# Optimization experiments

Hardware: AMD Instinct MI355X
Metric: run time of the kernel (lower is better)

Reference implementation:

```python
import jax, jax.numpy as jnp
import numpy as np

N = 50000
E = 800000
D_IN, D_HID, D_OUT = 256, 256, 128


def _xavier(key, shape):
    fan_in, fan_out = shape
    limit = float(np.sqrt(6.0 / (fan_in + fan_out)))
    return jax.random.uniform(key, shape, jnp.float32, -limit, limit)


def setup_inputs() -> dict:
    key = jax.random.key(0)
    ks = jax.random.split(key, 12)
    x = jax.random.normal(ks[0], (N, D_IN), jnp.float32)
    edge_index = jax.random.randint(ks[1], (2, E), 0, N, dtype=jnp.int64)
    batch = jnp.zeros((N,), jnp.int64)
    # per-layer: message weight W, linear weight LW (stored [in, out]), bias b
    w1 = _xavier(ks[2], (D_IN, D_HID))
    lw1 = _xavier(ks[3], (D_IN, D_HID))
    lb1 = jnp.zeros((D_HID,), jnp.float32)
    w2 = _xavier(ks[4], (D_HID, D_HID))
    lw2 = _xavier(ks[5], (D_HID, D_HID))
    lb2 = jnp.zeros((D_HID,), jnp.float32)
    w3 = _xavier(ks[6], (D_HID, D_OUT))
    lw3 = _xavier(ks[7], (D_HID, D_OUT))
    lb3 = jnp.zeros((D_OUT,), jnp.float32)
    return {"x": x, "edge_index": edge_index, "batch": batch,
            "w1": w1, "lw1": lw1, "lb1": lb1,
            "w2": w2, "lw2": lw2, "lb2": lb2,
            "w3": w3, "lw3": lw3, "lb3": lb3}


def _gcn_layer(x, W, LW, b, row, col, norm):
    # message: norm * (x_j @ W); equivalent and cheaper: transform nodes once, gather
    xw = x @ W                                   # [N, out]
    msg = norm[:, None] * xw[row]                # [E, out]
    agg = jax.ops.segment_sum(msg, col, num_segments=x.shape[0])  # scatter-add at col
    return agg + x @ LW + b                      # residual linear path


def reference(x, edge_index, batch, w1, lw1, lb1, w2, lw2, lb2, w3, lw3, lb3):
    row, col = edge_index[0], edge_index[1]
    ones = jnp.ones((row.shape[0],), x.dtype)
    out_deg = jax.ops.segment_sum(ones, row, num_segments=N)
    in_deg = jax.ops.segment_sum(ones, col, num_segments=N)
    # inf at zero-degree nodes never gets gathered (those nodes have no edges)
    norm = out_deg[row] ** -0.5 * in_deg[col] ** -0.5  # [E]

    h = jax.nn.relu(_gcn_layer(x, w1, lw1, lb1, row, col, norm))
    h = jax.nn.relu(_gcn_layer(h, w2, lw2, lb2, row, col, norm))
    h = jax.nn.sigmoid(_gcn_layer(h, w3, lw3, lb3, row, col, norm))
    return h
```

## Files before the change

kernel.cpp:

```cpp
#include <hip/hip_runtime.h>
#include <hip/hip_bf16.h>
#include <math.h>

#define NNODES 50000
#define NEDGES 800000
#define HNB 128
#define HBINS 50176
#define SCAN_NB 196

typedef short s8v __attribute__((ext_vector_type(8)));
typedef float f4v __attribute__((ext_vector_type(4)));
using bf16 = __hip_bfloat16;

static __device__ __forceinline__ float bf2f(unsigned int u16) {
    union { unsigned int i; float f; } c; c.i = u16 << 16; return c.f;
}


__global__ void k_packb(const float* __restrict__ W, const float* __restrict__ LW,
                        bf16* __restrict__ out, int K, int C) {
    int i = blockIdx.x * blockDim.x + threadIdx.x;
    int C2 = 2 * C;
    if (i >= K * C2) return;
    int k = i / C2, j = i % C2;
    float v = (j < C) ? W[k * C + j] : LW[k * C + (j - C)];
    out[i] = __float2bfloat16(v);
}


__global__ __launch_bounds__(256) void k_hist(const int* __restrict__ ei, ushort* __restrict__ partials) {
    __shared__ unsigned int h32[HBINS / 2];
    int b = blockIdx.x, row = blockIdx.y, t = threadIdx.x;
    for (int i = t; i < HBINS / 2; i += 256) h32[i] = 0;
    __syncthreads();
    const int chunk = NEDGES / HNB;
    int beg = b * chunk, end = beg + chunk;
    const int* p = ei + (size_t)row * NEDGES;
    for (int e = beg + t; e < end; e += 256) {
        int id = p[e];
        atomicAdd(&h32[id >> 1], 1u << (16 * (id & 1)));
    }
    __syncthreads();
    unsigned int* o32 = (unsigned int*)(partials + ((size_t)row * HNB + b) * HBINS);
    for (int i = t; i < HBINS / 2; i += 256) o32[i] = h32[i];
}

__global__ __launch_bounds__(256) void k_hist_reduce(const ushort* __restrict__ partials,
                                                     float* __restrict__ rsqrt_out,
                                                     int* __restrict__ in_cnt,
                                                     int* __restrict__ block_sums) {
    __shared__ int sm[256];
    int row = blockIdx.y;
    int i = blockIdx.x * 256 + threadIdx.x;
    const ushort* p = partials + (size_t)row * HNB * HBINS + i;
    int s = 0;
#pragma unroll 4
    for (int b = 0; b < HNB; ++b) s += p[(size_t)b * HBINS];
    if (row == 0) {
        if (i < NNODES) rsqrt_out[i] = rsqrtf((float)s);
    } else {
        if (i < NNODES) in_cnt[i] = s;
        sm[threadIdx.x] = s;
        __syncthreads();
        for (int off = 128; off > 0; off >>= 1) {
            if (threadIdx.x < off) sm[threadIdx.x] += sm[threadIdx.x + off];
            __syncthreads();
        }
        if (threadIdx.x == 0) block_sums[blockIdx.x] = sm[0];
    }
}


__global__ void k_scan_blocks(const int* __restrict__ block_sums, int* __restrict__ block_base, int nb) {
    __shared__ int s[256];
    int t = threadIdx.x;
    int v = (t < nb) ? block_sums[t] : 0;
    s[t] = v;
    __syncthreads();
    for (int off = 1; off < 256; off <<= 1) {
        int u = (t >= off) ? s[t - off] : 0;
        __syncthreads();
        s[t] += u;
        __syncthreads();
    }
    block_base[t] = s[t] - v;
}

__global__ void k_scan_final(const int* __restrict__ in_cnt, const int* __restrict__ block_base,
                             int* __restrict__ offsets, int* __restrict__ cursor) {
    __shared__ int s[256];
    int b = blockIdx.x, t = threadIdx.x;
    int i = b * 256 + t;
    int v = (i < NNODES) ? in_cnt[i] : 0;
    s[t] = v;
    __syncthreads();
    for (int off = 1; off < 256; off <<= 1) {
        int u = (t >= off) ? s[t - off] : 0;
        __syncthreads();
        s[t] += u;
        __syncthreads();
    }
    int excl = s[t] - v + block_base[b];
    if (i < NNODES) { offsets[i] = excl; cursor[i] = excl; }
    if (i == NNODES - 1) offsets[NNODES] = excl + v;
}

__global__ void k_scatter(const int* __restrict__ ei, int* __restrict__ cursor,
                          int* __restrict__ src_sorted) {
    int e = blockIdx.x * blockDim.x + threadIdx.x;
    if (e < NEDGES) {
        int r = ei[e], c = ei[NEDGES + e];
        int p = atomicAdd(&cursor[c], 1);
        src_sorted[p] = r;
    }
}

template<int D, int C2, int ACT>
__global__ void k_agg_fused(const bf16* __restrict__ xwcat, const int* __restrict__ offsets,
                            const int* __restrict__ src_sorted, const float* __restrict__ rsqrt_out,
                            const float* __restrict__ bias, void* __restrict__ out) {
    const int L = D / 8;
    const int G = 64 / L;
    int lane = threadIdx.x & 63;
    int v = blockIdx.x * (blockDim.x >> 6) + (threadIdx.x >> 6);
    if (v >= NNODES) return;
    int g = lane / L, sl = lane % L;

    float accA[8], accB[8];
#pragma unroll
    for (int c = 0; c < 8; ++c) { accA[c] = 0.f; accB[c] = 0.f; }

    int beg = offsets[v], end = offsets[v + 1];
    const ushort* base = (const ushort*)xwcat + sl * 8;
    for (int j = beg + g; j < end; j += 2 * G) {
        int s = src_sorted[j];
        float w = rsqrt_out[s];
        uint4 q = *(const uint4*)(base + (size_t)s * C2);
        accA[0] += w * bf2f(q.x & 0xffffu); accA[1] += w * bf2f(q.x >> 16);
        accA[2] += w * bf2f(q.y & 0xffffu); accA[3] += w * bf2f(q.y >> 16);
        accA[4] += w * bf2f(q.z & 0xffffu); accA[5] += w * bf2f(q.z >> 16);
        accA[6] += w * bf2f(q.w & 0xffffu); accA[7] += w * bf2f(q.w >> 16);
        int jB = j + G;
        if (jB < end) {
            int s2 = src_sorted[jB];
            float w2 = rsqrt_out[s2];
            uint4 p = *(const uint4*)(base + (size_t)s2 * C2);
            accB[0] += w2 * bf2f(p.x & 0xffffu); accB[1] += w2 * bf2f(p.x >> 16);
            accB[2] += w2 * bf2f(p.y & 0xffffu); accB[3] += w2 * bf2f(p.y >> 16);
            accB[4] += w2 * bf2f(p.z & 0xffffu); accB[5] += w2 * bf2f(p.z >> 16);
            accB[6] += w2 * bf2f(p.w & 0xffffu); accB[7] += w2 * bf2f(p.w >> 16);
        }
    }
#pragma unroll
    for (int c = 0; c < 8; ++c) accA[c] += accB[c];
#pragma unroll
    for (int d = 32; d >= L; d >>= 1) {
#pragma unroll
        for (int c = 0; c < 8; ++c) accA[c] += __shfl_down(accA[c], d, 64);
    }

    if (lane < L) {
        float sc = (end > beg) ? rsqrtf((float)(end - beg)) : 0.f;
        const ushort* lwp = (const ushort*)xwcat + (size_t)v * C2 + D + sl * 8;
        uint4 ql = *(const uint4*)lwp;
        const float* bp = bias + sl * 8;
        float4 b0 = *(const float4*)bp, b1 = *(const float4*)(bp + 4);
        float h[8];
        h[0] = accA[0] * sc + bf2f(ql.x & 0xffffu) + b0.x;
        h[1] = accA[1] * sc + bf2f(ql.x >> 16)     + b0.y;
        h[2] = accA[2] * sc + bf2f(ql.y & 0xffffu) + b0.z;
        h[3] = accA[3] * sc + bf2f(ql.y >> 16)     + b0.w;
        h[4] = accA[4] * sc + bf2f(ql.z & 0xffffu) + b1.x;
        h[5] = accA[5] * sc + bf2f(ql.z >> 16)     + b1.y;
        h[6] = accA[6] * sc + bf2f(ql.w & 0xffffu) + b1.z;
        h[7] = accA[7] * sc + bf2f(ql.w >> 16)     + b1.w;
        if (ACT == 1) {
            union { bf16 hh[8]; uint4 u; } o;
#pragma unroll
            for (int c = 0; c < 8; ++c) o.hh[c] = __float2bfloat16(fmaxf(h[c], 0.f));
            *(uint4*)((ushort*)out + (size_t)v * D + sl * 8) = o.u;
        } else {
            float r[8];
#pragma unroll
            for (int c = 0; c < 8; ++c) r[c] = 1.f / (1.f + expf(-h[c]));
            float* op = (float*)out + (size_t)v * D + sl * 8;
            *(float4*)op = (float4){r[0], r[1], r[2], r[3]};
            *(float4*)(op + 4) = (float4){r[4], r[5], r[6], r[7]};
        }
    }
}

template<int C2, bool A_BF16>
__global__ __launch_bounds__(256) void k_gemm_fused(const void* __restrict__ Aptr,
                                                    const bf16* __restrict__ B,
                                                    bf16* __restrict__ Out) {
    __shared__ bf16 As[64][40];
    __shared__ bf16 Bs[128][40];
    const int R = NNODES;
    int t = threadIdx.x;
    int wave = t >> 6, lane = t & 63;
    int r0 = blockIdx.x * 64;
    int n0 = blockIdx.y * 128;

    f4v acc[8];
#pragma unroll
    for (int i = 0; i < 8; ++i) acc[i] = (f4v){0.f, 0.f, 0.f, 0.f};

    int arow = t >> 2, aseg = t & 3;
    int bn = t & 127, bhalf = t >> 7;

    for (int k0 = 0; k0 < 256; k0 += 32) {
        {
            union { bf16 h[8]; uint4 v; } u;
            int gr = r0 + arow;
            if (gr < R) {
                if (A_BF16) {
                    const bf16* Ab = (const bf16*)Aptr;
                    u.v = *(const uint4*)(Ab + (size_t)gr * 256 + k0 + aseg * 8);
                } else {
                    const float* Af = (const float*)Aptr;
                    const float4* p = (const float4*)(Af + (size_t)gr * 256 + k0 + aseg * 8);
                    float4 f0 = p[0], f1 = p[1];
                    u.h[0] = __float2bfloat16(f0.x); u.h[1] = __float2bfloat16(f0.y);
                    u.h[2] = __float2bfloat16(f0.z); u.h[3] = __float2bfloat16(f0.w);
                    u.h[4] = __float2bfloat16(f1.x); u.h[5] = __float2bfloat16(f1.y);
                    u.h[6] = __float2bfloat16(f1.z); u.h[7] = __float2bfloat16(f1.w);
                }
            } else {
                u.v = (uint4){0, 0, 0, 0};
            }
            *(uint4*)&As[arow][aseg * 8] = u.v;
        }
        {
#pragma unroll
            for (int s8 = 0; s8 < 2; ++s8) {
                int kseg = bhalf * 2 + s8;
                union { bf16 h[8]; uint4 v; } u;
#pragma unroll
                for (int j = 0; j < 8; ++j)
                    u.h[j] = B[(size_t)(k0 + kseg * 8 + j) * C2 + n0 + bn];
                *(uint4*)&Bs[bn][kseg * 8] = u.v;
            }
        }
        __syncthreads();
        int m = wave * 16 + (lane & 15);
        int kq = (lane >> 4) * 8;
        s8v a = *(const s8v*)&As[m][kq];
#pragma unroll
        for (int nt = 0; nt < 8; ++nt) {
            s8v b = *(const s8v*)&Bs[nt * 16 + (lane & 15)][kq];
            acc[nt] = __builtin_amdgcn_mfma_f32_16x16x32_bf16(a, b, acc[nt], 0, 0, 0);
        }
        __syncthreads();
    }
#pragma unroll
    for (int nt = 0; nt < 8; ++nt) {
#pragma unroll
        for (int r = 0; r < 4; ++r) {
            int grow = r0 + wave * 16 + (lane >> 4) * 4 + r;
            int gcol = n0 + nt * 16 + (lane & 15);
            if (grow < R)
                Out[(size_t)grow * C2 + gcol] = __float2bfloat16(acc[nt][r]);
        }
    }
}


extern "C" void kernel_launch(void* const* d_in, const int* in_sizes, int n_in,
                              void* d_out, int out_size, void* d_ws, size_t ws_size,
                              hipStream_t stream) {
    const float* x   = (const float*)d_in[0];
    const int*   ei  = (const int*)d_in[1];
    const float* w1  = (const float*)d_in[3];
    const float* lw1 = (const float*)d_in[4];
    const float* lb1 = (const float*)d_in[5];
    const float* w2  = (const float*)d_in[6];
    const float* lw2 = (const float*)d_in[7];
    const float* lb2 = (const float*)d_in[8];
    const float* w3  = (const float*)d_in[9];
    const float* lw3 = (const float*)d_in[10];
    const float* lb3 = (const float*)d_in[11];
    float* out = (float*)d_out;

    char* ws = (char*)d_ws;
    size_t off = 0;
    auto alloc = [&](size_t bytes) -> void* {
        void* p = ws + off;
        off += (bytes + 255) & ~(size_t)255;
        return p;
    };
    int*    in_cnt     = (int*)alloc((size_t)HBINS * 4);
    float*  rsqrt_out  = (float*)alloc((size_t)HBINS * 4);
    int*    offsets    = (int*)alloc((size_t)(NNODES + 1) * 4);
    int*    cursor     = (int*)alloc((size_t)NNODES * 4);
    int*    block_sums = (int*)alloc((size_t)256 * 4);
    int*    block_base = (int*)alloc((size_t)256 * 4);
    ushort* partials   = (ushort*)alloc((size_t)2 * HNB * HBINS * 2);
    int*    src_sorted = (int*)alloc((size_t)NEDGES * 4);
    bf16*   wcat1      = (bf16*)alloc((size_t)256 * 512 * 2);
    bf16*   wcat2      = (bf16*)alloc((size_t)256 * 512 * 2);
    bf16*   wcat3      = (bf16*)alloc((size_t)256 * 256 * 2);
    bf16*   xwcat      = (bf16*)alloc((size_t)NNODES * 512 * 2);
    bf16*   h1         = (bf16*)alloc((size_t)NNODES * 256 * 2);
    bf16*   h2         = (bf16*)alloc((size_t)NNODES * 256 * 2);

    k_packb<<<512, 256, 0, stream>>>(w1, lw1, wcat1, 256, 256);
    k_packb<<<512, 256, 0, stream>>>(w2, lw2, wcat2, 256, 256);
    k_packb<<<256, 256, 0, stream>>>(w3, lw3, wcat3, 256, 128);

    k_hist<<<dim3(HNB, 2), 256, 0, stream>>>(ei, partials);
    k_hist_reduce<<<dim3(SCAN_NB, 2), 256, 0, stream>>>(partials, rsqrt_out, in_cnt, block_sums);
    k_scan_blocks<<<1, 256, 0, stream>>>(block_sums, block_base, SCAN_NB);
    k_scan_final<<<SCAN_NB, 256, 0, stream>>>(in_cnt, block_base, offsets, cursor);
    int eblocks = (NEDGES + 255) / 256;
    k_scatter<<<eblocks, 256, 0, stream>>>(ei, cursor, src_sorted);

    int gx = (NNODES + 63) / 64;
    int ablocks = NNODES / 4;

    k_gemm_fused<512, false><<<dim3(gx, 4), 256, 0, stream>>>(x, wcat1, xwcat);
    k_agg_fused<256, 512, 1><<<ablocks, 256, 0, stream>>>(xwcat, offsets, src_sorted, rsqrt_out, lb1, h1);
    k_gemm_fused<512, true><<<dim3(gx, 4), 256, 0, stream>>>(h1, wcat2, xwcat);
    k_agg_fused<256, 512, 1><<<ablocks, 256, 0, stream>>>(xwcat, offsets, src_sorted, rsqrt_out, lb2, h2);
    k_gemm_fused<256, true><<<dim3(gx, 2), 256, 0, stream>>>(h2, wcat3, xwcat);
    k_agg_fused<128, 256, 2><<<ablocks, 256, 0, stream>>>(xwcat, offsets, src_sorted, rsqrt_out, lb3, out);
}
```

Baseline: 457.3 us.

## Preload neighbor ids per wave and unroll gather with shuffle broadcast

The aggregation kernel now runs one 64-thread wave per node. Each lane loads up to 64 neighbor ids and their weights once, then broadcasts them with shuffles inside a 4-way unrolled gather loop, with a scalar tail loop for degrees above 64. This removes the serialized dependent index-then-weight loads from the inner loop and adds memory-level parallelism. The bf16 high-half unpack now uses a mask instead of a shift. In exchange it launches many small blocks and does wasted predicated loads (weight zero, reading row of id 0) when the degree is not a multiple of the unrolled stride.

```diff
diff --git a/kernel.cpp b/kernel.cpp
--- a/kernel.cpp
+++ b/kernel.cpp
@@ -12,8 +12,11 @@
 typedef float f4v __attribute__((ext_vector_type(4)));
 using bf16 = __hip_bfloat16;
 
-static __device__ __forceinline__ float bf2f(unsigned int u16) {
-    union { unsigned int i; float f; } c; c.i = u16 << 16; return c.f;
+static __device__ __forceinline__ float bflo(unsigned int x) {
+    union { unsigned int i; float f; } c; c.i = x << 16; return c.f;
+}
+static __device__ __forceinline__ float bfhi(unsigned int x) {
+    union { unsigned int i; float f; } c; c.i = x & 0xffff0000u; return c.f;
 }
 
 
@@ -116,64 +119,84 @@
 }
 
 template<int D, int C2, int ACT>
-__global__ void k_agg_fused(const bf16* __restrict__ xwcat, const int* __restrict__ offsets,
-                            const int* __restrict__ src_sorted, const float* __restrict__ rsqrt_out,
-                            const float* __restrict__ bias, void* __restrict__ out) {
+__global__ __launch_bounds__(64) void k_agg_fused(const bf16* __restrict__ xwcat,
+                                                  const int* __restrict__ offsets,
+                                                  const int* __restrict__ src_sorted,
+                                                  const float* __restrict__ rsqrt_out,
+                                                  const float* __restrict__ bias,
+                                                  void* __restrict__ out) {
     const int L = D / 8;
     const int G = 64 / L;
-    int lane = threadIdx.x & 63;
-    int v = blockIdx.x * (blockDim.x >> 6) + (threadIdx.x >> 6);
-    if (v >= NNODES) return;
+    const int U = 4;
+    int lane = threadIdx.x;
+    int v = blockIdx.x;
     int g = lane / L, sl = lane % L;
 
-    float accA[8], accB[8];
-#pragma unroll
-    for (int c = 0; c < 8; ++c) { accA[c] = 0.f; accB[c] = 0.f; }
-
     int beg = offsets[v], end = offsets[v + 1];
+    int deg = end - beg;
+    int dcap = min(deg, 64);
+
+    int id = 0; float wl = 0.f;
+    if (lane < dcap) {
+        id = src_sorted[beg + lane];
+        wl = rsqrt_out[id];
+    }
+
+    float acc[U][8];
+#pragma unroll
+    for (int u = 0; u < U; ++u)
+#pragma unroll
+        for (int c = 0; c < 8; ++c) acc[u][c] = 0.f;
+
     const ushort* base = (const ushort*)xwcat + sl * 8;
-    for (int j = beg + g; j < end; j += 2 * G) {
+
+    for (int e0 = 0; e0 < dcap; e0 += G * U) {
+#pragma unroll
+        for (int u = 0; u < U; ++u) {
+            int e = e0 + u * G + g;
+            int s = __shfl(id, e & 63, 64);
+            float w = __shfl(wl, e & 63, 64);
+            if (e >= dcap) w = 0.f;
+            uint4 q = *(const uint4*)(base + (size_t)s * C2);
+            acc[u][0] += w * bflo(q.x); acc[u][1] += w * bfhi(q.x);
+            acc[u][2] += w * bflo(q.y); acc[u][3] += w * bfhi(q.y);
+            acc[u][4] += w * bflo(q.z); acc[u][5] += w * bfhi(q.z);
+            acc[u][6] += w * bflo(q.w); acc[u][7] += w * bfhi(q.w);
+        }
+    }
+    for (int j = beg + 64 + g; j < end; j += G) {
         int s = src_sorted[j];
         float w = rsqrt_out[s];
         uint4 q = *(const uint4*)(base + (size_t)s * C2);
-        accA[0] += w * bf2f(q.x & 0xffffu); accA[1] += w * bf2f(q.x >> 16);
-        accA[2] += w * bf2f(q.y & 0xffffu); accA[3] += w * bf2f(q.y >> 16);
-        accA[4] += w * bf2f(q.z & 0xffffu); accA[5] += w * bf2f(q.z >> 16);
-        accA[6] += w * bf2f(q.w & 0xffffu); accA[7] += w * bf2f(q.w >> 16);
-        int jB = j + G;
-        if (jB < end) {
-            int s2 = src_sorted[jB];
-            float w2 = rsqrt_out[s2];
-            uint4 p = *(const uint4*)(base + (size_t)s2 * C2);
-            accB[0] += w2 * bf2f(p.x & 0xffffu); accB[1] += w2 * bf2f(p.x >> 16);
-            accB[2] += w2 * bf2f(p.y & 0xffffu); accB[3] += w2 * bf2f(p.y >> 16);
-            accB[4] += w2 * bf2f(p.z & 0xffffu); accB[5] += w2 * bf2f(p.z >> 16);
-            accB[6] += w2 * bf2f(p.w & 0xffffu); accB[7] += w2 * bf2f(p.w >> 16);
-        }
-    }
-#pragma unroll
-    for (int c = 0; c < 8; ++c) accA[c] += accB[c];
+        acc[0][0] += w * bflo(q.x); acc[0][1] += w * bfhi(q.x);
+        acc[0][2] += w * bflo(q.y); acc[0][3] += w * bfhi(q.y);
+        acc[0][4] += w * bflo(q.z); acc[0][5] += w * bfhi(q.z);
+        acc[0][6] += w * bflo(q.w); acc[0][7] += w * bfhi(q.w);
+    }
+
+#pragma unroll
+    for (int c = 0; c < 8; ++c) acc[0][c] = (acc[0][c] + acc[1][c]) + (acc[2][c] + acc[3][c]);
 #pragma unroll
     for (int d = 32; d >= L; d >>= 1) {
 #pragma unroll
-        for (int c = 0; c < 8; ++c) accA[c] += __shfl_down(accA[c], d, 64);
+        for (int c = 0; c < 8; ++c) acc[0][c] += __shfl_down(acc[0][c], d, 64);
     }
 
     if (lane < L) {
-        float sc = (end > beg) ? rsqrtf((float)(end - beg)) : 0.f;
+        float sc = (deg > 0) ? rsqrtf((float)deg) : 0.f;
         const ushort* lwp = (const ushort*)xwcat + (size_t)v * C2 + D + sl * 8;
         uint4 ql = *(const uint4*)lwp;
         const float* bp = bias + sl * 8;
         float4 b0 = *(const float4*)bp, b1 = *(const float4*)(bp + 4);
         float h[8];
-        h[0] = accA[0] * sc + bf2f(ql.x & 0xffffu) + b0.x;
-        h[1] = accA[1] * sc + bf2f(ql.x >> 16)     + b0.y;
-        h[2] = accA[2] * sc + bf2f(ql.y & 0xffffu) + b0.z;
-        h[3] = accA[3] * sc + bf2f(ql.y >> 16)     + b0.w;
-        h[4] = accA[4] * sc + bf2f(ql.z & 0xffffu) + b1.x;
-        h[5] = accA[5] * sc + bf2f(ql.z >> 16)     + b1.y;
-        h[6] = accA[6] * sc + bf2f(ql.w & 0xffffu) + b1.z;
-        h[7] = accA[7] * sc + bf2f(ql.w >> 16)     + b1.w;
+        h[0] = acc[0][0] * sc + bflo(ql.x) + b0.x;
+        h[1] = acc[0][1] * sc + bfhi(ql.x) + b0.y;
+        h[2] = acc[0][2] * sc + bflo(ql.y) + b0.z;
+        h[3] = acc[0][3] * sc + bfhi(ql.y) + b0.w;
+        h[4] = acc[0][4] * sc + bflo(ql.z) + b1.x;
+        h[5] = acc[0][5] * sc + bfhi(ql.z) + b1.y;
+        h[6] = acc[0][6] * sc + bflo(ql.w) + b1.z;
+        h[7] = acc[0][7] * sc + bfhi(ql.w) + b1.w;
         if (ACT == 1) {
             union { bf16 hh[8]; uint4 u; } o;
 #pragma unroll
@@ -316,12 +339,11 @@
     k_scatter<<<eblocks, 256, 0, stream>>>(ei, cursor, src_sorted);
 
     int gx = (NNODES + 63) / 64;
-    int ablocks = NNODES / 4;
 
     k_gemm_fused<512, false><<<dim3(gx, 4), 256, 0, stream>>>(x, wcat1, xwcat);
-    k_agg_fused<256, 512, 1><<<ablocks, 256, 0, stream>>>(xwcat, offsets, src_sorted, rsqrt_out, lb1, h1);
+    k_agg_fused<256, 512, 1><<<NNODES, 64, 0, stream>>>(xwcat, offsets, src_sorted, rsqrt_out, lb1, h1);
     k_gemm_fused<512, true><<<dim3(gx, 4), 256, 0, stream>>>(h1, wcat2, xwcat);
-    k_agg_fused<256, 512, 1><<<ablocks, 256, 0, stream>>>(xwcat, offsets, src_sorted, rsqrt_out, lb2, h2);
+    k_agg_fused<256, 512, 1><<<NNODES, 64, 0, stream>>>(xwcat, offsets, src_sorted, rsqrt_out, lb2, h2);
     k_gemm_fused<256, true><<<dim3(gx, 2), 256, 0, stream>>>(h2, wcat3, xwcat);
-    k_agg_fused<128, 256, 2><<<ablocks, 256, 0, stream>>>(xwcat, offsets, src_sorted, rsqrt_out, lb3, out);
-}
+    k_agg_fused<128, 256, 2><<<NNODES, 64, 0, stream>>>(xwcat, offsets, src_sorted, rsqrt_out, lb3, out);
+}
```

Result: faster. 440.7 us (-3.6%).
